# Optimization experiments

Hardware: AMD Instinct MI355X
Metric: run time of the kernel (lower is better)

The kernel has to match this reference:

```python
import jax, jax.numpy as jnp
import numpy as np

B, S, E, H = 4, 2048, 1024, 16
DK = E // H

def setup_inputs() -> dict:
    key = jax.random.key(0)
    ks = jax.random.split(key, 5)
    scale = 1.0 / np.sqrt(E)
    return {
        "x":  jax.random.normal(ks[0], (B, S, E), dtype=jnp.float32),
        "Wq": jax.random.normal(ks[1], (E, E), dtype=jnp.float32) * scale,
        "Wk": jax.random.normal(ks[2], (E, E), dtype=jnp.float32) * scale,
        "Wv": jax.random.normal(ks[3], (E, E), dtype=jnp.float32) * scale,
        "Wo": jax.random.normal(ks[4], (E, E), dtype=jnp.float32) * scale,
    }

def reference(x, Wq, Wk, Wv, Wo):
    b, s, e = x.shape
    # nn.Linear (no bias): y = x @ W.T
    def split_heads(t):  # (b, s, e) -> (b, H, s, DK)
        return t.reshape(b, s, H, DK).transpose(0, 2, 1, 3)
    Q = split_heads(x @ Wq.T)
    K = split_heads(x @ Wk.T)
    V = split_heads(x @ Wv.T)
    scores = jnp.einsum('bhqd,bhkd->bhqk', Q, K) / jnp.sqrt(jnp.float32(DK))
    attn = jax.nn.softmax(scores, axis=-1)  # dropout p=0.0 -> identity
    ctx = jnp.einsum('bhqk,bhkd->bhqd', attn, V)
    concat = ctx.transpose(0, 2, 1, 3).reshape(b, s, e)
    return concat @ Wo.T
```

## Files before the change

### kernel.cpp

```cpp
#include <hip/hip_runtime.h>


typedef __bf16 bf16x8 __attribute__((ext_vector_type(8)));
typedef __bf16 bf16x4 __attribute__((ext_vector_type(4)));
typedef float floatx4 __attribute__((ext_vector_type(4)));

#define GLOAD_LDS16(gp, lp) __builtin_amdgcn_global_load_lds( \
    (const __attribute__((address_space(1))) unsigned int*)(gp), \
    (__attribute__((address_space(3))) unsigned int*)(lp), 16, 0, 0)

__global__ __launch_bounds__(256) void cvt_x(const float4* __restrict__ s,
                                             bf16x4* __restrict__ d, int n4) {
    int i = blockIdx.x * 256 + threadIdx.x;
    if (i < n4) {
        float4 v = s[i];
        bf16x4 o = { (__bf16)v.x, (__bf16)v.y, (__bf16)v.z, (__bf16)v.w };
        d[i] = o;
    }
}

__global__ __launch_bounds__(256) void cvt_w(const float4* __restrict__ Wq,
                                             const float4* __restrict__ Wk,
                                             const float4* __restrict__ Wv,
                                             const float4* __restrict__ Wo,
                                             bf16x4* __restrict__ oq, bf16x4* __restrict__ ok,
                                             bf16x4* __restrict__ ov, bf16x4* __restrict__ oo,
                                             float qscale) {
    int y = blockIdx.y;
    const float4* s = (y == 0) ? Wq : (y == 1) ? Wk : (y == 2) ? Wv : Wo;
    bf16x4* d = (y == 0) ? oq : (y == 1) ? ok : (y == 2) ? ov : oo;
    float scale = (y == 0) ? qscale : 1.0f;
    int i = blockIdx.x * 256 + threadIdx.x;
    float4 v = s[i];
    bf16x4 o = { (__bf16)(v.x * scale), (__bf16)(v.y * scale),
                 (__bf16)(v.z * scale), (__bf16)(v.w * scale) };
    d[i] = o;
}


__device__ __forceinline__ void gemm_stage(const __bf16* __restrict__ A,
                                           const __bf16* __restrict__ W,
                                           __bf16* Asm, __bf16* Bsm,
                                           int bm, int bn, int k0, int w, int lane) {
#pragma unroll
    for (int j = 0; j < 2; ++j) {
        int base = j * 256 + w * 64;
        int flat = base + lane;
        int c = flat >> 7, r = flat & 127;
        GLOAD_LDS16(A + (size_t)(bm + r) * 1024 + k0 + c * 8, (char*)Asm + base * 16);
    }
#pragma unroll
    for (int j = 0; j < 4; ++j) {
        int base = j * 256 + w * 64;
        int flat = base + lane;
        int c = flat >> 8, r = flat & 255;
        GLOAD_LDS16(W + (size_t)(bn + r) * 1024 + k0 + c * 8, (char*)Bsm + base * 16);
    }
}

__device__ __forceinline__ void gemm_phase(const __bf16* __restrict__ A,
                                           const __bf16* __restrict__ W,
                                           const __bf16* Asm_r, const __bf16* Bsm_r,
                                           __bf16* Asm_s, __bf16* Bsm_s,
                                           int bm, int bn, int ks,
                                           int w, int lane, int quad, int l15,
                                           int wy, int wx,
                                           floatx4 acc[4][8]) {
    gemm_stage(A, W, Asm_s, Bsm_s, bm, bn, ks, w, lane);
    __builtin_amdgcn_sched_barrier(0);
    asm volatile("s_waitcnt vmcnt(6)" ::: "memory");
    __builtin_amdgcn_s_barrier();
    __builtin_amdgcn_sched_barrier(0);

    bf16x8 af[4], bf[8];
#pragma unroll
    for (int mt = 0; mt < 4; ++mt)
        af[mt] = *(const bf16x8*)(Asm_r + (quad * 128 + wy * 64 + mt * 16 + l15) * 8);
#pragma unroll
    for (int nt = 0; nt < 8; ++nt)
        bf[nt] = *(const bf16x8*)(Bsm_r + (quad * 256 + wx * 128 + nt * 16 + l15) * 8);
#pragma unroll
    for (int mt = 0; mt < 4; ++mt)
#pragma unroll
        for (int nt = 0; nt < 8; ++nt)
            acc[mt][nt] = __builtin_amdgcn_mfma_f32_16x16x32_bf16(af[mt], bf[nt],
                                                                  acc[mt][nt], 0, 0, 0);
    __builtin_amdgcn_sched_barrier(0);
    __builtin_amdgcn_s_barrier();
}

__device__ __forceinline__ void gemm_mainloop2(const __bf16* __restrict__ A,
                                               const __bf16* __restrict__ W,
                                               __bf16* SM,
                                               int bm, int bn, int tid,
                                               floatx4 acc[4][8]) {
    const int w = tid >> 6, lane = tid & 63;
    const int quad = lane >> 4, l15 = lane & 15;
    const int wy = w >> 1, wx = w & 1;
    __bf16* Asm0 = SM;
    __bf16* Bsm0 = SM + 4096;
    __bf16* Asm1 = SM + 12288;
    __bf16* Bsm1 = SM + 16384;
#pragma unroll
    for (int i = 0; i < 4; ++i)
#pragma unroll
        for (int j = 0; j < 8; ++j) acc[i][j] = (floatx4){0.f, 0.f, 0.f, 0.f};

    gemm_stage(A, W, Asm0, Bsm0, bm, bn, 0, w, lane);

    for (int k0 = 0; k0 < 1024; k0 += 64) {
        gemm_phase(A, W, Asm0, Bsm0, Asm1, Bsm1, bm, bn, k0 + 32,
                   w, lane, quad, l15, wy, wx, acc);
        gemm_phase(A, W, Asm1, Bsm1, Asm0, Bsm0, bm, bn, k0 + 64,
                   w, lane, quad, l15, wy, wx, acc);
    }
    __syncthreads();
}

__global__ __launch_bounds__(256, 2) void gemm_qkv(const __bf16* __restrict__ A,
                                                   const __bf16* __restrict__ Wqb,
                                                   const __bf16* __restrict__ Wkb,
                                                   const __bf16* __restrict__ Wvb,
                                                   __bf16* __restrict__ Qg,
                                                   __bf16* __restrict__ Kg,
                                                   __bf16* __restrict__ Vtg) {
    __shared__ alignas(16) __bf16 SM[24576];
    const int sel = blockIdx.x >> 2;
    const __bf16* W = (sel == 0) ? Wqb : (sel == 1) ? Wkb : Wvb;
    __bf16* ob = (sel == 0) ? Qg : (sel == 1) ? Kg : Vtg;
    const int bm = blockIdx.y * 128, bn = (blockIdx.x & 3) * 256;
    const int tid = threadIdx.x;
    const int w = tid >> 6, lane = tid & 63;
    const int quad = lane >> 4, l15 = lane & 15;
    const int wy = w >> 1, wx = w & 1;

    floatx4 acc[4][8];
    gemm_mainloop2(A, W, SM, bm, bn, tid, acc);

    float* tb = (float*)SM + w * 272;
    const int rr = lane >> 2, c0 = (lane & 3) * 4;
#pragma unroll
    for (int mt = 0; mt < 4; ++mt)
#pragma unroll
        for (int nt = 0; nt < 8; ++nt) {
            if (sel == 2) {
#pragma unroll
                for (int r = 0; r < 4; ++r) tb[l15 * 17 + quad * 4 + r] = acc[mt][nt][r];
            } else {
#pragma unroll
                for (int r = 0; r < 4; ++r) tb[(quad * 4 + r) * 17 + l15] = acc[mt][nt][r];
            }
            float f0 = tb[rr * 17 + c0 + 0], f1 = tb[rr * 17 + c0 + 1];
            float f2 = tb[rr * 17 + c0 + 2], f3 = tb[rr * 17 + c0 + 3];
            bf16x4 pk = { (__bf16)f0, (__bf16)f1, (__bf16)f2, (__bf16)f3 };
            if (sel <= 1) {
                int m = bm + wy * 64 + mt * 16 + rr;
                int n0 = bn + wx * 128 + nt * 16 + c0;
                int bI = m >> 11, s = m & 2047, h = n0 >> 6, d0 = n0 & 63;
                *(bf16x4*)(ob + ((size_t)(bI * 16 + h) * 2048 + s) * 64 + d0) = pk;
            } else {
                int m0 = bm + wy * 64 + mt * 16 + c0;
                int n = bn + wx * 128 + nt * 16 + rr;
                int bI = m0 >> 11, s0 = m0 & 2047, h = n >> 6, d = n & 63;
                *(bf16x4*)(ob + ((size_t)(bI * 16 + h) * 64 + d) * 2048 + s0) = pk;
            }
        }
}

__global__ __launch_bounds__(256, 2) void gemm_out(const __bf16* __restrict__ A,
                                                   const __bf16* __restrict__ W,
                                                   float* __restrict__ of) {
    __shared__ alignas(16) __bf16 SM[24576];
    const int tid = threadIdx.x;
    const int lane = tid & 63, w = tid >> 6;
    const int quad = lane >> 4, l15 = lane & 15;
    const int wy = w >> 1, wx = w & 1;
    const int bm = blockIdx.y * 128, bn = blockIdx.x * 256;

    floatx4 acc[4][8];
    gemm_mainloop2(A, W, SM, bm, bn, tid, acc);

#pragma unroll
    for (int mt = 0; mt < 4; ++mt)
#pragma unroll
        for (int nt = 0; nt < 8; ++nt)
#pragma unroll
            for (int r = 0; r < 4; ++r) {
                int m = bm + wy * 64 + mt * 16 + quad * 4 + r;
                int n = bn + wx * 128 + nt * 16 + l15;
                of[(size_t)m * 1024 + n] = acc[mt][nt][r];
            }
}


__device__ __forceinline__ int paddr(int c, int row) {
    int r2 = row ^ (((row >> 3) & 1) << 1) ^ (c & 1);
    return (c * 32 + r2) * 16;
}

__device__ __forceinline__ void attn_stage(const __bf16* __restrict__ Kg,
                                           const __bf16* __restrict__ Vtg,
                                           __bf16* Ks, __bf16* Vs,
                                           int bh, int kv0, int w, int lane) {
#pragma unroll
    for (int j = 0; j < 2; ++j) {
        int base = j * 256 + w * 64;
        int flat = base + lane;
        int c = flat >> 6, r = flat & 63;
        GLOAD_LDS16(Kg + ((size_t)bh * 2048 + kv0 + r) * 64 + c * 8, (char*)Ks + base * 16);
        GLOAD_LDS16(Vtg + ((size_t)bh * 64 + r) * 2048 + kv0 + c * 8, (char*)Vs + base * 16);
    }
}

__device__ __forceinline__ void attn_phase(const __bf16* __restrict__ Kg,
                                           const __bf16* __restrict__ Vtg,
                                           const __bf16* Ksr, const __bf16* Vsr,
                                           __bf16* Kss, __bf16* Vss,
                                           char* Pw, const bf16x8 qf[2][2],
                                           int bh, int kv_next,
                                           int w, int lane, int quad, int l15,
                                           float l_p[2][4], floatx4 o[2][4]) {
    attn_stage(Kg, Vtg, Kss, Vss, bh, kv_next * 64, w, lane);
    __builtin_amdgcn_sched_barrier(0);
    asm volatile("s_waitcnt vmcnt(4)" ::: "memory");
    __builtin_amdgcn_s_barrier();
    __builtin_amdgcn_sched_barrier(0);

    floatx4 sa[2][4];
#pragma unroll
    for (int mt = 0; mt < 2; ++mt)
#pragma unroll
        for (int nt = 0; nt < 4; ++nt) sa[mt][nt] = (floatx4){0.f, 0.f, 0.f, 0.f};
#pragma unroll
    for (int nt = 0; nt < 4; ++nt) {
        bf16x8 kb0 = *(const bf16x8*)(Ksr + (quad * 64 + nt * 16 + l15) * 8);
        bf16x8 kb1 = *(const bf16x8*)(Ksr + ((4 + quad) * 64 + nt * 16 + l15) * 8);
#pragma unroll
        for (int mt = 0; mt < 2; ++mt) {
            sa[mt][nt] = __builtin_amdgcn_mfma_f32_16x16x32_bf16(qf[mt][0], kb0,
                                                                sa[mt][nt], 0, 0, 0);
            sa[mt][nt] = __builtin_amdgcn_mfma_f32_16x16x32_bf16(qf[mt][1], kb1,
                                                                sa[mt][nt], 0, 0, 0);
        }
    }

#pragma unroll
    for (int mt = 0; mt < 2; ++mt)
#pragma unroll
        for (int nt = 0; nt < 4; ++nt)
#pragma unroll
            for (int r = 0; r < 4; ++r) {
                float p = __builtin_amdgcn_exp2f(sa[mt][nt][r]);
                l_p[mt][r] += p;
                unsigned u = __builtin_bit_cast(unsigned, p);
                *(unsigned short*)(Pw + paddr(nt * 2 + (l15 >> 3),
                                              mt * 16 + quad * 4 + r)
                                   + (l15 & 7) * 2) = (unsigned short)(u >> 16);
            }

#pragma unroll
    for (int kk = 0; kk < 2; ++kk) {
        bf16x8 pa0 = *(const bf16x8*)(Pw + paddr(kk * 4 + quad, l15));
        bf16x8 pa1 = *(const bf16x8*)(Pw + paddr(kk * 4 + quad, 16 + l15));
#pragma unroll
        for (int dt = 0; dt < 4; ++dt) {
            bf16x8 vb = *(const bf16x8*)(Vsr + ((kk * 4 + quad) * 64 + dt * 16 + l15) * 8);
            o[0][dt] = __builtin_amdgcn_mfma_f32_16x16x32_bf16(pa0, vb, o[0][dt], 0, 0, 0);
            o[1][dt] = __builtin_amdgcn_mfma_f32_16x16x32_bf16(pa1, vb, o[1][dt], 0, 0, 0);
        }
    }
    __builtin_amdgcn_sched_barrier(0);
    __builtin_amdgcn_s_barrier();
}

__global__ __launch_bounds__(256, 3) void attn_kernel(const __bf16* __restrict__ Qg,
                                                      const __bf16* __restrict__ Kg,
                                                      const __bf16* __restrict__ Vtg,
                                                      __bf16* __restrict__ ctxg) {
    __shared__ alignas(16) __bf16 Ksm0[4096];
    __shared__ alignas(16) __bf16 Vsm0[4096];
    __shared__ alignas(16) __bf16 Ksm1[4096];
    __shared__ alignas(16) __bf16 Vsm1[4096];
    __shared__ alignas(16) __bf16 Psm[8192];
    const int tid = threadIdx.x;
    const int w = tid >> 6, lane = tid & 63;
    const int quad = lane >> 4, l15 = lane & 15;

    const int orig = blockIdx.x;
    const int wg = (orig & 7) * 128 + (orig >> 3);
    const int qbase = (wg & 15) * 128;
    const int bh = wg >> 4;

    char* Pw = (char*)Psm + w * 4096;

    bf16x8 qf[2][2];
#pragma unroll
    for (int mt = 0; mt < 2; ++mt) {
        const __bf16* qrow = Qg + ((size_t)bh * 2048 + qbase + w * 32 + mt * 16 + l15) * 64;
        qf[mt][0] = *(const bf16x8*)(qrow + quad * 8);
        qf[mt][1] = *(const bf16x8*)(qrow + 32 + quad * 8);
    }

    float l_p[2][4] = {{0.f, 0.f, 0.f, 0.f}, {0.f, 0.f, 0.f, 0.f}};
    floatx4 o[2][4];
#pragma unroll
    for (int mt = 0; mt < 2; ++mt)
#pragma unroll
        for (int dt = 0; dt < 4; ++dt) o[mt][dt] = (floatx4){0.f, 0.f, 0.f, 0.f};

    attn_stage(Kg, Vtg, Ksm0, Vsm0, bh, 0, w, lane);

    for (int kv = 0; kv < 32; kv += 2) {
        attn_phase(Kg, Vtg, Ksm0, Vsm0, Ksm1, Vsm1, Pw, qf, bh, kv + 1,
                   w, lane, quad, l15, l_p, o);
        attn_phase(Kg, Vtg, Ksm1, Vsm1, Ksm0, Vsm0, Pw, qf, bh, (kv + 2) & 31,
                   w, lane, quad, l15, l_p, o);
    }

    __syncthreads();

    float inv[2][4];
#pragma unroll
    for (int mt = 0; mt < 2; ++mt)
#pragma unroll
        for (int r = 0; r < 4; ++r) {
            float t = l_p[mt][r];
            t += __shfl_xor(t, 1); t += __shfl_xor(t, 2);
            t += __shfl_xor(t, 4); t += __shfl_xor(t, 8);
            inv[mt][r] = 1.f / t;
        }

    float* tb = (float*)Ksm0 + w * 272;
    const int bI = bh >> 4, h = bh & 15;
    const int rr = lane >> 2, c0 = (lane & 3) * 4;
#pragma unroll
    for (int mt = 0; mt < 2; ++mt)
#pragma unroll
        for (int dt = 0; dt < 4; ++dt) {
#pragma unroll
            for (int r = 0; r < 4; ++r)
                tb[(quad * 4 + r) * 17 + l15] = o[mt][dt][r] * inv[mt][r];
            float f0 = tb[rr * 17 + c0 + 0], f1 = tb[rr * 17 + c0 + 1];
            float f2 = tb[rr * 17 + c0 + 2], f3 = tb[rr * 17 + c0 + 3];
            bf16x4 pk = { (__bf16)f0, (__bf16)f1, (__bf16)f2, (__bf16)f3 };
            *(bf16x4*)(ctxg + ((size_t)(bI * 2048 + qbase + w * 32 + mt * 16 + rr)) * 1024
                       + h * 64 + dt * 16 + c0) = pk;
        }
}

extern "C" void kernel_launch(void* const* d_in, const int* in_sizes, int n_in,
                              void* d_out, int out_size, void* d_ws, size_t ws_size,
                              hipStream_t stream) {
    const float* x  = (const float*)d_in[0];
    const float* Wq = (const float*)d_in[1];
    const float* Wk = (const float*)d_in[2];
    const float* Wv = (const float*)d_in[3];
    const float* Wo = (const float*)d_in[4];
    float* out = (float*)d_out;
    char* ws = (char*)d_ws;

    __bf16* xb  = (__bf16*)(ws);
    __bf16* wqb = (__bf16*)(ws + (16u << 20));
    __bf16* wkb = (__bf16*)(ws + (18u << 20));
    __bf16* wvb = (__bf16*)(ws + (20u << 20));
    __bf16* wob = (__bf16*)(ws + (22u << 20));
    __bf16* Qg  = (__bf16*)(ws + (24u << 20));
    __bf16* Kg  = (__bf16*)(ws + (40u << 20));
    __bf16* Vtg = (__bf16*)(ws + (56u << 20));
    __bf16* ctx = xb;

    const float qscale = 0.18033688011112042f;

    cvt_x<<<8192, 256, 0, stream>>>((const float4*)x, (bf16x4*)xb, 2097152);
    cvt_w<<<dim3(1024, 4), 256, 0, stream>>>((const float4*)Wq, (const float4*)Wk,
                                             (const float4*)Wv, (const float4*)Wo,
                                             (bf16x4*)wqb, (bf16x4*)wkb,
                                             (bf16x4*)wvb, (bf16x4*)wob, qscale);

    gemm_qkv<<<dim3(12, 64), 256, 0, stream>>>(xb, wqb, wkb, wvb, Qg, Kg, Vtg);

    attn_kernel<<<1024, 256, 0, stream>>>(Qg, Kg, Vtg, ctx);

    gemm_out<<<dim3(4, 64), 256, 0, stream>>>(ctx, wob, out);
}
```

Baseline: 309.9 us.

## Triple-buffer GEMM k-loop and transpose QK^T MFMA for packed P stores

The projection GEMMs move from a two-stage to a three-stage LDS ring with two tiles in flight, and the wait count is relaxed so loads overlap compute over a longer window. This raises LDS use to 72 KB per block, which may reduce occupancy under the launch bound of 2. In attention, the QK^T MFMA operands are swapped so each lane holds four consecutive keys for one query row. P can then be packed into bf16 pairs with perm and written as 8-byte stores instead of scalar 16-bit stores, and the row-sum reduction becomes a per-lane scalar with a two-step shuffle.

```diff
diff --git a/kernel.cpp b/kernel.cpp
--- a/kernel.cpp
+++ b/kernel.cpp
@@ -4,6 +4,7 @@
 typedef __bf16 bf16x8 __attribute__((ext_vector_type(8)));
 typedef __bf16 bf16x4 __attribute__((ext_vector_type(4)));
 typedef float floatx4 __attribute__((ext_vector_type(4)));
+typedef unsigned int uint2v __attribute__((ext_vector_type(2)));
 
 #define GLOAD_LDS16(gp, lp) __builtin_amdgcn_global_load_lds( \
     (const __attribute__((address_space(1))) unsigned int*)(gp), \
@@ -68,7 +69,7 @@
                                            floatx4 acc[4][8]) {
     gemm_stage(A, W, Asm_s, Bsm_s, bm, bn, ks, w, lane);
     __builtin_amdgcn_sched_barrier(0);
-    asm volatile("s_waitcnt vmcnt(6)" ::: "memory");
+    asm volatile("s_waitcnt vmcnt(12)" ::: "memory");
     __builtin_amdgcn_s_barrier();
     __builtin_amdgcn_sched_barrier(0);
 
@@ -89,7 +90,7 @@
     __builtin_amdgcn_s_barrier();
 }
 
-__device__ __forceinline__ void gemm_mainloop2(const __bf16* __restrict__ A,
+__device__ __forceinline__ void gemm_mainloop3(const __bf16* __restrict__ A,
                                                const __bf16* __restrict__ W,
                                                __bf16* SM,
                                                int bm, int bn, int tid,
@@ -97,23 +98,28 @@
     const int w = tid >> 6, lane = tid & 63;
     const int quad = lane >> 4, l15 = lane & 15;
     const int wy = w >> 1, wx = w & 1;
-    __bf16* Asm0 = SM;
-    __bf16* Bsm0 = SM + 4096;
-    __bf16* Asm1 = SM + 12288;
-    __bf16* Bsm1 = SM + 16384;
+    __bf16* As[3] = { SM, SM + 12288, SM + 24576 };
+    __bf16* Bs[3] = { SM + 4096, SM + 16384, SM + 28672 };
 #pragma unroll
     for (int i = 0; i < 4; ++i)
 #pragma unroll
         for (int j = 0; j < 8; ++j) acc[i][j] = (floatx4){0.f, 0.f, 0.f, 0.f};
 
-    gemm_stage(A, W, Asm0, Bsm0, bm, bn, 0, w, lane);
-
-    for (int k0 = 0; k0 < 1024; k0 += 64) {
-        gemm_phase(A, W, Asm0, Bsm0, Asm1, Bsm1, bm, bn, k0 + 32,
+    gemm_stage(A, W, As[0], Bs[0], bm, bn, 0, w, lane);
+    gemm_stage(A, W, As[1], Bs[1], bm, bn, 32, w, lane);
+
+    for (int t = 0; t < 30; t += 3) {
+        gemm_phase(A, W, As[0], Bs[0], As[2], Bs[2], bm, bn, (t + 2) * 32,
                    w, lane, quad, l15, wy, wx, acc);
-        gemm_phase(A, W, Asm1, Bsm1, Asm0, Bsm0, bm, bn, k0 + 64,
+        gemm_phase(A, W, As[1], Bs[1], As[0], Bs[0], bm, bn, (t + 3) * 32,
                    w, lane, quad, l15, wy, wx, acc);
-    }
+        gemm_phase(A, W, As[2], Bs[2], As[1], Bs[1], bm, bn, (t + 4) * 32,
+                   w, lane, quad, l15, wy, wx, acc);
+    }
+    gemm_phase(A, W, As[0], Bs[0], As[2], Bs[2], bm, bn, 1024,
+               w, lane, quad, l15, wy, wx, acc);
+    gemm_phase(A, W, As[1], Bs[1], As[0], Bs[0], bm, bn, 1056,
+               w, lane, quad, l15, wy, wx, acc);
     __syncthreads();
 }
 
@@ -124,7 +130,7 @@
                                                    __bf16* __restrict__ Qg,
                                                    __bf16* __restrict__ Kg,
                                                    __bf16* __restrict__ Vtg) {
-    __shared__ alignas(16) __bf16 SM[24576];
+    __shared__ alignas(16) __bf16 SM[36864];
     const int sel = blockIdx.x >> 2;
     const __bf16* W = (sel == 0) ? Wqb : (sel == 1) ? Wkb : Wvb;
     __bf16* ob = (sel == 0) ? Qg : (sel == 1) ? Kg : Vtg;
@@ -135,7 +141,7 @@
     const int wy = w >> 1, wx = w & 1;
 
     floatx4 acc[4][8];
-    gemm_mainloop2(A, W, SM, bm, bn, tid, acc);
+    gemm_mainloop3(A, W, SM, bm, bn, tid, acc);
 
     float* tb = (float*)SM + w * 272;
     const int rr = lane >> 2, c0 = (lane & 3) * 4;
@@ -170,7 +176,7 @@
 __global__ __launch_bounds__(256, 2) void gemm_out(const __bf16* __restrict__ A,
                                                    const __bf16* __restrict__ W,
                                                    float* __restrict__ of) {
-    __shared__ alignas(16) __bf16 SM[24576];
+    __shared__ alignas(16) __bf16 SM[36864];
     const int tid = threadIdx.x;
     const int lane = tid & 63, w = tid >> 6;
     const int quad = lane >> 4, l15 = lane & 15;
@@ -178,7 +184,7 @@
     const int bm = blockIdx.y * 128, bn = blockIdx.x * 256;
 
     floatx4 acc[4][8];
-    gemm_mainloop2(A, W, SM, bm, bn, tid, acc);
+    gemm_mainloop3(A, W, SM, bm, bn, tid, acc);
 
 #pragma unroll
     for (int mt = 0; mt < 4; ++mt)
@@ -219,7 +225,7 @@
                                            char* Pw, const bf16x8 qf[2][2],
                                            int bh, int kv_next,
                                            int w, int lane, int quad, int l15,
-                                           float l_p[2][4], floatx4 o[2][4]) {
+                                           float l_p[2], floatx4 o[2][4]) {
     attn_stage(Kg, Vtg, Kss, Vss, bh, kv_next * 64, w, lane);
     __builtin_amdgcn_sched_barrier(0);
     asm volatile("s_waitcnt vmcnt(4)" ::: "memory");
@@ -237,9 +243,9 @@
         bf16x8 kb1 = *(const bf16x8*)(Ksr + ((4 + quad) * 64 + nt * 16 + l15) * 8);
 #pragma unroll
         for (int mt = 0; mt < 2; ++mt) {
-            sa[mt][nt] = __builtin_amdgcn_mfma_f32_16x16x32_bf16(qf[mt][0], kb0,
+            sa[mt][nt] = __builtin_amdgcn_mfma_f32_16x16x32_bf16(kb0, qf[mt][0],
                                                                 sa[mt][nt], 0, 0, 0);
-            sa[mt][nt] = __builtin_amdgcn_mfma_f32_16x16x32_bf16(qf[mt][1], kb1,
+            sa[mt][nt] = __builtin_amdgcn_mfma_f32_16x16x32_bf16(kb1, qf[mt][1],
                                                                 sa[mt][nt], 0, 0, 0);
         }
     }
@@ -247,16 +253,22 @@
 #pragma unroll
     for (int mt = 0; mt < 2; ++mt)
 #pragma unroll
-        for (int nt = 0; nt < 4; ++nt)
-#pragma unroll
-            for (int r = 0; r < 4; ++r) {
-                float p = __builtin_amdgcn_exp2f(sa[mt][nt][r]);
-                l_p[mt][r] += p;
-                unsigned u = __builtin_bit_cast(unsigned, p);
-                *(unsigned short*)(Pw + paddr(nt * 2 + (l15 >> 3),
-                                              mt * 16 + quad * 4 + r)
-                                   + (l15 & 7) * 2) = (unsigned short)(u >> 16);
-            }
+        for (int nt = 0; nt < 4; ++nt) {
+            float p0 = __builtin_amdgcn_exp2f(sa[mt][nt][0]);
+            float p1 = __builtin_amdgcn_exp2f(sa[mt][nt][1]);
+            float p2 = __builtin_amdgcn_exp2f(sa[mt][nt][2]);
+            float p3 = __builtin_amdgcn_exp2f(sa[mt][nt][3]);
+            l_p[mt] += (p0 + p1) + (p2 + p3);
+            unsigned u0 = __builtin_bit_cast(unsigned, p0);
+            unsigned u1 = __builtin_bit_cast(unsigned, p1);
+            unsigned u2 = __builtin_bit_cast(unsigned, p2);
+            unsigned u3 = __builtin_bit_cast(unsigned, p3);
+            uint2v pk;
+            pk.x = __builtin_amdgcn_perm(u1, u0, 0x07060302);
+            pk.y = __builtin_amdgcn_perm(u3, u2, 0x07060302);
+            *(uint2v*)(Pw + paddr(nt * 2 + (quad >> 1), mt * 16 + l15)
+                       + (quad & 1) * 8) = pk;
+        }
 
 #pragma unroll
     for (int kk = 0; kk < 2; ++kk) {
@@ -301,7 +313,7 @@
         qf[mt][1] = *(const bf16x8*)(qrow + 32 + quad * 8);
     }
 
-    float l_p[2][4] = {{0.f, 0.f, 0.f, 0.f}, {0.f, 0.f, 0.f, 0.f}};
+    float l_p[2] = {0.f, 0.f};
     floatx4 o[2][4];
 #pragma unroll
     for (int mt = 0; mt < 2; ++mt)
@@ -319,16 +331,22 @@
 
     __syncthreads();
 
-    float inv[2][4];
-#pragma unroll
-    for (int mt = 0; mt < 2; ++mt)
-#pragma unroll
-        for (int r = 0; r < 4; ++r) {
-            float t = l_p[mt][r];
-            t += __shfl_xor(t, 1); t += __shfl_xor(t, 2);
-            t += __shfl_xor(t, 4); t += __shfl_xor(t, 8);
-            inv[mt][r] = 1.f / t;
-        }
+    float invr[2][4];
+    {
+        float inv[2];
+#pragma unroll
+        for (int mt = 0; mt < 2; ++mt) {
+            float t = l_p[mt];
+            t += __shfl_xor(t, 16);
+            t += __shfl_xor(t, 32);
+            inv[mt] = 1.f / t;
+        }
+#pragma unroll
+        for (int mt = 0; mt < 2; ++mt)
+#pragma unroll
+            for (int r = 0; r < 4; ++r)
+                invr[mt][r] = __shfl(inv[mt], quad * 4 + r);
+    }
 
     float* tb = (float*)Ksm0 + w * 272;
     const int bI = bh >> 4, h = bh & 15;
@@ -339,7 +357,7 @@
         for (int dt = 0; dt < 4; ++dt) {
 #pragma unroll
             for (int r = 0; r < 4; ++r)
-                tb[(quad * 4 + r) * 17 + l15] = o[mt][dt][r] * inv[mt][r];
+                tb[(quad * 4 + r) * 17 + l15] = o[mt][dt][r] * invr[mt][r];
             float f0 = tb[rr * 17 + c0 + 0], f1 = tb[rr * 17 + c0 + 1];
             float f2 = tb[rr * 17 + c0 + 2], f3 = tb[rr * 17 + c0 + 3];
             bf16x4 pk = { (__bf16)f0, (__bf16)f1, (__bf16)f2, (__bf16)f3 };
```

Result: slower. 322.3 us (+4.0%).
